# Kernel optimization log

Hardware: AMD Instinct MI355X
Metric: run time of the kernel (lower is better)

Reference implementation:

```python
import jax, jax.numpy as jnp
import numpy as np

N = 16384      # total ligand atoms
E = 65536      # edges
B = 256        # graphs / batch
MAXN = 64      # atoms per graph (max_nodes for to_dense_batch)
FIN = 64       # num_node_features
HID = 256      # hidden_channels
GH = 2         # gat heads
LP = 1024      # protein length
NH = 4         # cross-attention heads
HD = HID // NH
VOCAB = 22


def setup_inputs() -> dict:
    key = jax.random.key(0)
    ks = jax.random.split(key, 48)
    f = jnp.float32
    def nrm(k, shape, s=0.05):
        return jax.random.normal(k, shape, f) * s
    inp = {}
    inp["x"] = jax.random.normal(ks[0], (N, FIN), f)
    inp["edge_index"] = jax.random.randint(ks[1], (2, E), 0, N)
    inp["batch"] = jnp.arange(N) // MAXN  # sorted, 64 atoms per graph
    inp["protein_seq"] = jax.random.randint(ks[2], (B, LP), 0, VOCAB)
    # GAT layer 1 (FIN -> HID, GH heads, concat=False)
    inp["w1"] = nrm(ks[3], (FIN, GH * HID)); inp["as1"] = nrm(ks[4], (GH, HID)); inp["ad1"] = nrm(ks[5], (GH, HID)); inp["b1"] = jnp.zeros((HID,), f)
    inp["w2"] = nrm(ks[6], (HID, GH * HID)); inp["as2"] = nrm(ks[7], (GH, HID)); inp["ad2"] = nrm(ks[8], (GH, HID)); inp["b2"] = jnp.zeros((HID,), f)
    inp["w3"] = nrm(ks[9], (HID, GH * HID)); inp["as3"] = nrm(ks[10], (GH, HID)); inp["ad3"] = nrm(ks[11], (GH, HID)); inp["b3"] = jnp.zeros((HID,), f)
    # protein embedding + conv1d (OIH layout)
    inp["emb"] = nrm(ks[12], (VOCAB, HID), 0.1)
    inp["conv_w"] = nrm(ks[13], (HID, HID, 3)); inp["conv_b"] = jnp.zeros((HID,), f)
    # cross-attention MHA
    inp["wq"] = nrm(ks[14], (HID, HID)); inp["bq"] = jnp.zeros((HID,), f)
    inp["wk"] = nrm(ks[15], (HID, HID)); inp["bk"] = jnp.zeros((HID,), f)
    inp["wv"] = nrm(ks[16], (HID, HID)); inp["bv"] = jnp.zeros((HID,), f)
    inp["wo"] = nrm(ks[17], (HID, HID)); inp["bo"] = jnp.zeros((HID,), f)
    inp["ln1_g"] = jnp.ones((HID,), f); inp["ln1_b"] = jnp.zeros((HID,), f)
    inp["ffw1"] = nrm(ks[18], (HID, 4 * HID)); inp["ffb1"] = jnp.zeros((4 * HID,), f)
    inp["ffw2"] = nrm(ks[19], (4 * HID, HID)); inp["ffb2"] = jnp.zeros((HID,), f)
    inp["ln2_g"] = jnp.ones((HID,), f); inp["ln2_b"] = jnp.zeros((HID,), f)
    inp["fc1_w"] = nrm(ks[20], (HID, HID)); inp["fc1_b"] = jnp.zeros((HID,), f)
    inp["fc2_w"] = nrm(ks[21], (HID, 1)); inp["fc2_b"] = jnp.zeros((1,), f)
    return inp


def _gat(x, edge_index, W, a_src, a_dst, bias):
    # PyG GATConv, concat=False (mean over heads), add_self_loops=True
    n = x.shape[0]
    h = (x @ W).reshape(n, GH, HID)                      # [N,GH,C]
    loop = jnp.arange(n)
    src = jnp.concatenate([edge_index[0], loop])
    dst = jnp.concatenate([edge_index[1], loop])
    a_s = jnp.einsum('nhc,hc->nh', h, a_src)             # [N,GH]
    a_d = jnp.einsum('nhc,hc->nh', h, a_dst)
    e = jax.nn.leaky_relu(a_s[src] + a_d[dst], 0.2)      # [E+N,GH]
    emax = jax.ops.segment_max(e, dst, num_segments=n)   # each node has a self-loop
    ex = jnp.exp(e - emax[dst])
    den = jax.ops.segment_sum(ex, dst, num_segments=n)
    alpha = ex / den[dst]                                # [E+N,GH]
    msg = h[src] * alpha[:, :, None]
    out = jax.ops.segment_sum(msg, dst, num_segments=n)  # [N,GH,C]
    return out.mean(axis=1) + bias


def _to_dense_batch(x, batch):
    # batch is sorted node->graph ids; counts per graph <= MAXN
    ones = jnp.ones((x.shape[0],), jnp.int32)
    counts = jax.ops.segment_sum(ones, batch, num_segments=B)
    starts = jnp.cumsum(counts) - counts
    pos = jnp.arange(x.shape[0]) - starts[batch]
    dense = jnp.zeros((B, MAXN, x.shape[1]), x.dtype).at[batch, pos].set(x)
    mask = jnp.zeros((B, MAXN), bool).at[batch, pos].set(True)
    return dense, mask


def _layernorm(x, g, b, eps=1e-5):
    mu = x.mean(-1, keepdims=True)
    var = ((x - mu) ** 2).mean(-1, keepdims=True)
    return (x - mu) * jax.lax.rsqrt(var + eps) * g + b


def reference(x, edge_index, batch, protein_seq,
              w1, as1, ad1, b1, w2, as2, ad2, b2, w3, as3, ad3, b3,
              emb, conv_w, conv_b,
              wq, bq, wk, bk, wv, bv, wo, bo,
              ln1_g, ln1_b, ffw1, ffb1, ffw2, ffb2, ln2_g, ln2_b,
              fc1_w, fc1_b, fc2_w, fc2_b):
    # --- ligand GNN (eval mode: dropout = identity) ---
    h = jax.nn.elu(_gat(x, edge_index, w1, as1, ad1, b1))
    h = jax.nn.elu(_gat(h, edge_index, w2, as2, ad2, b2))
    h = jax.nn.elu(_gat(h, edge_index, w3, as3, ad3, b3))
    lig, lig_mask = _to_dense_batch(h, batch)            # [B,MAXN,HID], [B,MAXN]
    # --- protein branch ---
    p = emb[protein_seq]                                 # [B,LP,HID]
    p = p.transpose(0, 2, 1)                             # [B,HID,LP]
    p = jax.lax.conv_general_dilated(p, conv_w, (1,), [(1, 1)],
                                     dimension_numbers=('NCH', 'OIH', 'NCH'))
    p = jax.nn.relu(p + conv_b[None, :, None]).transpose(0, 2, 1)  # [B,LP,HID]
    kpm = protein_seq == 0                               # key padding mask
    # --- cross attention (query=ligand, key/value=protein) ---
    q = (lig @ wq + bq).reshape(B, MAXN, NH, HD)
    k = (p @ wk + bk).reshape(B, LP, NH, HD)
    v = (p @ wv + bv).reshape(B, LP, NH, HD)
    scores = jnp.einsum('bqhd,bkhd->bhqk', q, k) / np.sqrt(HD).astype(np.float32)
    scores = jnp.where(kpm[:, None, None, :], jnp.float32(-1e9), scores)
    attn = jax.nn.softmax(scores, axis=-1)               # [B,NH,MAXN,LP]
    ctx = jnp.einsum('bhqk,bkhd->bqhd', attn, v).reshape(B, MAXN, HID)
    attn_out = ctx @ wo + bo
    y = _layernorm(lig + attn_out, ln1_g, ln1_b)
    ff = jax.nn.gelu(y @ ffw1 + ffb1, approximate=False) @ ffw2 + ffb2
    y = _layernorm(y + ff, ln2_g, ln2_b)
    # --- masked mean pool ---
    m = lig_mask[:, :, None].astype(y.dtype)
    pooled = (y * m).sum(axis=1) / (m.sum(axis=1) + 1e-6)
    out = jax.nn.relu(pooled @ fc1_w + fc1_b)
    return out @ fc2_w + fc2_b                           # [B,1]
```

## Files before the change

### kernel.cpp

```cpp
#include <hip/hip_runtime.h>
#include <hip/hip_bf16.h>
#include <cstdint>
#include <cstddef>

#define NAT 16384
#define NED 65536
#define BGR 256
#define FIN 64
#define HID 256
#define LPN 1024
#define HD 64
#define NTRIP 11638
#define NTAB  11648

typedef __bf16 bf16x8 __attribute__((ext_vector_type(8)));
typedef float floatx4 __attribute__((ext_vector_type(4)));

__device__ __forceinline__ void gl2lds16(const void* g, void* l)
{
    __builtin_amdgcn_global_load_lds(
        (const __attribute__((address_space(1))) unsigned int*)g,
        (__attribute__((address_space(3))) unsigned int*)l, 16, 0, 0);
}

template<int ACT, int OUTBF16, int BIASROW>
__global__ __launch_bounds__(512) void gemm_mfma(const __bf16* __restrict__ A,
    const __bf16* __restrict__ Bt, const float* __restrict__ bias,
    void* __restrict__ Cout, int M, int Nn, int K, float escale)
{
    __shared__ __bf16 As[2][128][32];
    __shared__ __bf16 Bs[2][128][32];
    const int t = threadIdx.x;
    const int m0 = blockIdx.y * 128, n0 = blockIdx.x * 128;
    const int w = t >> 6, lane = t & 63;
    const int wm = (w & 3) * 32, wn = (w >> 2) * 64;
    const int quad = lane >> 4, l16 = lane & 15;
    const int r0 = t >> 2, s0 = t & 3, g0 = (s0 ^ (r0 & 3)) * 8;
    const int fso = (quad ^ (l16 & 3)) * 8;
    floatx4 acc[2][4] = {};
    for (int k0 = 0; k0 < K; k0 += 64) {
        gl2lds16(A + (size_t)(m0 + r0) * K + k0 + g0,       &As[0][r0][s0 * 8]);
        gl2lds16(A + (size_t)(m0 + r0) * K + k0 + 32 + g0,  &As[1][r0][s0 * 8]);
        gl2lds16(Bt + (size_t)(n0 + r0) * K + k0 + g0,      &Bs[0][r0][s0 * 8]);
        gl2lds16(Bt + (size_t)(n0 + r0) * K + k0 + 32 + g0, &Bs[1][r0][s0 * 8]);
        __syncthreads();
#pragma unroll
        for (int c = 0; c < 2; c++) {
            bf16x8 af[2], bfr[4];
#pragma unroll
            for (int mi = 0; mi < 2; mi++) af[mi]  = *(const bf16x8*)&As[c][wm + mi * 16 + l16][fso];
#pragma unroll
            for (int nj = 0; nj < 4; nj++) bfr[nj] = *(const bf16x8*)&Bs[c][wn + nj * 16 + l16][fso];
#pragma unroll
            for (int mi = 0; mi < 2; mi++)
#pragma unroll
                for (int nj = 0; nj < 4; nj++)
                    acc[mi][nj] = __builtin_amdgcn_mfma_f32_16x16x32_bf16(af[mi], bfr[nj], acc[mi][nj], 0, 0, 0);
        }
        __syncthreads();
    }
#pragma unroll
    for (int mi = 0; mi < 2; mi++)
#pragma unroll
        for (int nj = 0; nj < 4; nj++) {
            int col = n0 + wn + nj * 16 + l16;
#pragma unroll
            for (int r = 0; r < 4; r++) {
                int row = m0 + wm + mi * 16 + quad * 4 + r;
                float bval = bias ? (BIASROW ? bias[row] : bias[col]) : 0.f;
                float v = (acc[mi][nj][r] + bval) * escale;
                if (ACT == 1) v = fmaxf(v, 0.f);
                if (ACT == 2) v = 0.5f * v * (1.f + erff(v * 0.70710678118654752f));
                if (OUTBF16) ((__bf16*)Cout)[(size_t)row * Nn + col] = (__bf16)v;
                else         ((float*)Cout)[(size_t)row * Nn + col] = v;
            }
        }
}

__global__ __launch_bounds__(512) void gemm_gat(const __bf16* __restrict__ A,
    const __bf16* __restrict__ Bt, const float* __restrict__ as_f,
    const float* __restrict__ ad_f, __bf16* __restrict__ Hg,
    float* __restrict__ part, int K)
{
    __shared__ __bf16 As[2][128][32];
    __shared__ __bf16 Bs[2][128][32];
    const int t = threadIdx.x;
    const int m0 = blockIdx.y * 128, n0 = blockIdx.x * 128;
    const int w = t >> 6, lane = t & 63;
    const int wm = (w & 3) * 32, wn = (w >> 2) * 64;
    const int quad = lane >> 4, l16 = lane & 15;
    const int r0 = t >> 2, s0 = t & 3, g0 = (s0 ^ (r0 & 3)) * 8;
    const int fso = (quad ^ (l16 & 3)) * 8;
    floatx4 acc[2][4] = {};
    for (int k0 = 0; k0 < K; k0 += 64) {
        gl2lds16(A + (size_t)(m0 + r0) * K + k0 + g0,       &As[0][r0][s0 * 8]);
        gl2lds16(A + (size_t)(m0 + r0) * K + k0 + 32 + g0,  &As[1][r0][s0 * 8]);
        gl2lds16(Bt + (size_t)(n0 + r0) * K + k0 + g0,      &Bs[0][r0][s0 * 8]);
        gl2lds16(Bt + (size_t)(n0 + r0) * K + k0 + 32 + g0, &Bs[1][r0][s0 * 8]);
        __syncthreads();
#pragma unroll
        for (int c = 0; c < 2; c++) {
            bf16x8 af[2], bfr[4];
#pragma unroll
            for (int mi = 0; mi < 2; mi++) af[mi]  = *(const bf16x8*)&As[c][wm + mi * 16 + l16][fso];
#pragma unroll
            for (int nj = 0; nj < 4; nj++) bfr[nj] = *(const bf16x8*)&Bs[c][wn + nj * 16 + l16][fso];
#pragma unroll
            for (int mi = 0; mi < 2; mi++)
#pragma unroll
                for (int nj = 0; nj < 4; nj++)
                    acc[mi][nj] = __builtin_amdgcn_mfma_f32_16x16x32_bf16(af[mi], bfr[nj], acc[mi][nj], 0, 0, 0);
        }
        __syncthreads();
    }
    const int slot = blockIdx.x * 2 + (w >> 2);
#pragma unroll
    for (int mi = 0; mi < 2; mi++) {
#pragma unroll
        for (int r = 0; r < 4; r++) {
            float ps = 0.f, pd = 0.f;
#pragma unroll
            for (int nj = 0; nj < 4; nj++) {
                int col = n0 + wn + nj * 16 + l16;
                float v = acc[mi][nj][r];
                ps += v * as_f[col];
                pd += v * ad_f[col];
            }
#pragma unroll
            for (int off = 1; off < 16; off <<= 1) {
                ps += __shfl_xor(ps, off, 64);
                pd += __shfl_xor(pd, off, 64);
            }
            if (l16 == 0) {
                int row = m0 + wm + mi * 16 + quad * 4 + r;
                part[(size_t)(slot * 2 + 0) * NAT + row] = ps;
                part[(size_t)(slot * 2 + 1) * NAT + row] = pd;
            }
        }
    }
#pragma unroll
    for (int mi = 0; mi < 2; mi++)
#pragma unroll
        for (int nj = 0; nj < 4; nj++) {
            int col = n0 + wn + nj * 16 + l16;
#pragma unroll
            for (int r = 0; r < 4; r++) {
                int row = m0 + wm + mi * 16 + quad * 4 + r;
                Hg[(size_t)row * 512 + col] = (__bf16)acc[mi][nj][r];
            }
        }
}

__global__ void fold_k(const float* __restrict__ part, float* __restrict__ a_s,
                       float* __restrict__ a_d)
{
    int n = blockIdx.x * 256 + threadIdx.x;
    float s0 = 0.f, d0 = 0.f, s1 = 0.f, d1 = 0.f;
#pragma unroll
    for (int sl = 0; sl < 4; sl++) {
        s0 += part[(size_t)(sl * 2 + 0) * NAT + n];
        d0 += part[(size_t)(sl * 2 + 1) * NAT + n];
        s1 += part[(size_t)((sl + 4) * 2 + 0) * NAT + n];
        d1 += part[(size_t)((sl + 4) * 2 + 1) * NAT + n];
    }
    a_s[n * 2 + 0] = s0; a_s[n * 2 + 1] = s1;
    a_d[n * 2 + 0] = d0; a_d[n * 2 + 1] = d1;
}

__global__ __launch_bounds__(256) void tap_k(const float* __restrict__ emb,
    const float* __restrict__ cw, float* __restrict__ tap)
{
    const int dlv = blockIdx.x >> 2, part = blockIdx.x & 3;
    const int dl = dlv / 22, v = dlv % 22;
    const int n = threadIdx.x;
    const float* er = emb + v * 256 + part * 64;
    const float* wr = cw + (size_t)n * 768 + part * 192 + dl;
    float s = 0.f;
    for (int k = 0; k < 64; k += 4) {
        s += er[k + 0] * wr[k * 3 + 0];
        s += er[k + 1] * wr[k * 3 + 3];
        s += er[k + 2] * wr[k * 3 + 6];
        s += er[k + 3] * wr[k * 3 + 9];
    }
    atomicAdd(&tap[(size_t)dlv * 256 + n], s);
}

__global__ __launch_bounds__(256) void ptab_k(const float* __restrict__ tap,
    const float* __restrict__ bias, __bf16* __restrict__ P)
{
    const int t = threadIdx.x;
    const int row = blockIdx.x * 8 + (t >> 5);
    const int c = (t & 31) * 8;
    __bf16 o[8];
    if (row < NTRIP) {
        const int a = row / 506, rem = row - a * 506;
        const int t1 = rem / 23, c2 = rem - t1 * 23;
        float acc[8];
#pragma unroll
        for (int j = 0; j < 8; j++) acc[j] = bias[c + j];
        if (a > 0) {
            const float* r = tap + (size_t)(0 * 22 + (a - 1)) * 256 + c;
#pragma unroll
            for (int j = 0; j < 8; j++) acc[j] += r[j];
        }
        {
            const float* r = tap + (size_t)(1 * 22 + t1) * 256 + c;
#pragma unroll
            for (int j = 0; j < 8; j++) acc[j] += r[j];
        }
        if (c2 > 0) {
            const float* r = tap + (size_t)(2 * 22 + (c2 - 1)) * 256 + c;
#pragma unroll
            for (int j = 0; j < 8; j++) acc[j] += r[j];
        }
#pragma unroll
        for (int j = 0; j < 8; j++) o[j] = (__bf16)fmaxf(acc[j], 0.f);
    } else {
#pragma unroll
        for (int j = 0; j < 8; j++) o[j] = (__bf16)0.f;
    }
    *(uint4*)(P + (size_t)row * 256 + c) = *(uint4*)o;
}

__global__ void tid_k(const int* __restrict__ seq, unsigned short* __restrict__ tid)
{
    int i = blockIdx.x * 256 + threadIdx.x;
    int b = i >> 10, l = i & 1023;
    const int* sr = seq + b * LPN;
    int t0 = (l > 0) ? sr[l - 1] : -1;
    int t1 = sr[l];
    int t2 = (l < LPN - 1) ? sr[l + 1] : -1;
    int v = (t0 + 1) * 506 + t1 * 23 + (t2 + 1);
    tid[i] = (unsigned short)(v | (t1 == 0 ? 0x8000 : 0));
}

struct Segs {
    const float* src[12];
    __bf16* dst[12];
    int kdim[12];
    int ndim[12];
    int mode[12];
    int start[13];
};

__global__ void cvtall_k(Segs S, int total)
{
    int i = blockIdx.x * 256 + threadIdx.x;
    if (i >= total) return;
    int s = 0;
    while (i >= S.start[s + 1]) s++;
    int j = i - S.start[s];
    if (S.mode[s] == 0) {
        S.dst[s][j] = (__bf16)S.src[s][j];
    } else {
        int K = S.kdim[s], N = S.ndim[s];
        int n = j / K, k = j - n * K;
        S.dst[s][j] = (__bf16)S.src[s][(size_t)k * N + n];
    }
}

__global__ void deg_k(const int* __restrict__ ei, int* __restrict__ deg)
{
    int e = blockIdx.x * 256 + threadIdx.x;
    if (e < NED) atomicAdd(&deg[ei[NED + e]], 1);
}

__global__ __launch_bounds__(256) void scan_k(const int* __restrict__ deg, int* __restrict__ rowptr)
{
    __shared__ int part[256];
    int t = threadIdx.x;
    int base = t * 64;
    int s = 0;
#pragma unroll
    for (int i = 0; i < 64; i++) s += deg[base + i];
    part[t] = s;
    __syncthreads();
    for (int off = 1; off < 256; off <<= 1) {
        int v = (t >= off) ? part[t - off] : 0;
        __syncthreads();
        part[t] += v;
        __syncthreads();
    }
    int run = t ? part[t - 1] : 0;
    for (int i = 0; i < 64; i++) { rowptr[base + i] = run; run += deg[base + i]; }
    if (t == 255) rowptr[16384] = run;
}

__global__ void scat_k(const int* __restrict__ ei, int* __restrict__ fill,
                       const int* __restrict__ rowptr, int* __restrict__ csrc,
                       int* __restrict__ cdst)
{
    int e = blockIdx.x * 256 + threadIdx.x;
    if (e >= NED) return;
    int d = ei[NED + e];
    int pos = rowptr[d] + atomicAdd(&fill[d], 1);
    csrc[pos] = ei[e];
    cdst[pos] = d;
}

__global__ void erec_k(const int* __restrict__ csrc, const int* __restrict__ cdst,
    const float* __restrict__ a_s, const float* __restrict__ a_d,
    float4* __restrict__ rec)
{
    int p = blockIdx.x * 256 + threadIdx.x;
    if (p >= NED) return;
    int s = csrc[p], d = cdst[p];
    float2 as2 = *(const float2*)(a_s + s * 2);
    float2 ad2 = *(const float2*)(a_d + d * 2);
    float e0 = as2.x + ad2.x; e0 = (e0 > 0.f) ? e0 : 0.2f * e0;
    float e1 = as2.y + ad2.y; e1 = (e1 > 0.f) ? e1 : 0.2f * e1;
    rec[p] = make_float4(e0, e1, __int_as_float(s), 0.f);
}

__global__ __launch_bounds__(256) void gat_agg(const int* __restrict__ rowptr,
    const float4* __restrict__ rec, const __bf16* __restrict__ hgb,
    const float* __restrict__ a_s, const float* __restrict__ a_d,
    const float* __restrict__ bias, float* __restrict__ out, __bf16* __restrict__ outb)
{
    const int wave = threadIdx.x >> 6, lane = threadIdx.x & 63;
    const int d = blockIdx.x * 4 + wave;
    const int beg = rowptr[d], end = rowptr[d + 1];
    float2 as2 = *(const float2*)(a_s + d * 2);
    float2 ad2 = *(const float2*)(a_d + d * 2);
    float e0 = as2.x + ad2.x; e0 = (e0 > 0.f) ? e0 : 0.2f * e0;
    float e1 = as2.y + ad2.y; e1 = (e1 > 0.f) ? e1 : 0.2f * e1;
    float m0 = e0, den0 = 1.f, m1 = e1, den1 = 1.f;
    for (int p = beg; p < end; p++) {
        float4 rc = rec[p];
        float nm0 = fmaxf(m0, rc.x);
        den0 = den0 * __expf(m0 - nm0) + __expf(rc.x - nm0);
        m0 = nm0;
        float nm1 = fmaxf(m1, rc.y);
        den1 = den1 * __expf(m1 - nm1) + __expf(rc.y - nm1);
        m1 = nm1;
    }
    const float inv0 = 1.f / den0, inv1 = 1.f / den1;
    const int ch = lane * 8;
    const int g = ch >> 8;
    const float mg = g ? m1 : m0, invg = g ? inv1 : inv0;
    float acc[8] = {};
    {
        float al = __expf((g ? e1 : e0) - mg) * invg;
        bf16x8 hv = *(const bf16x8*)(hgb + (size_t)d * 512 + ch);
#pragma unroll
        for (int j = 0; j < 8; j++) acc[j] += (float)hv[j] * al;
    }
    for (int p = beg; p < end; p++) {
        float4 rc = rec[p];
        float al = __expf((g ? rc.y : rc.x) - mg) * invg;
        int s = __float_as_int(rc.z);
        bf16x8 hv = *(const bf16x8*)(hgb + (size_t)s * 512 + ch);
#pragma unroll
        for (int j = 0; j < 8; j++) acc[j] += (float)hv[j] * al;
    }
    float other[8];
#pragma unroll
    for (int j = 0; j < 8; j++) other[j] = __shfl_xor(acc[j], 32, 64);
    if (lane < 32) {
#pragma unroll
        for (int j = 0; j < 8; j++) {
            float v = 0.5f * (acc[j] + other[j]) + bias[ch + j];
            v = (v > 0.f) ? v : expm1f(v);
            if (out) out[(size_t)d * 256 + ch + j] = v;
            outb[(size_t)d * 256 + ch + j] = (__bf16)v;
        }
    }
}

__global__ __launch_bounds__(256) void attn4_k(const __bf16* __restrict__ Qb,
    const __bf16* __restrict__ Ktab, const __bf16* __restrict__ Vtab,
    const unsigned short* __restrict__ tid16, __bf16* __restrict__ O)
{
    __shared__ __bf16 Vs[2][4096];
    __shared__ __bf16 Ps[4][16][72];
    __shared__ unsigned short tids[1024];
    const int t = threadIdx.x;
    const int b = blockIdx.x >> 2, h = blockIdx.x & 3;
    const int w = t >> 6, lane = t & 63;
    const int quad = lane >> 4, l16 = lane & 15;
    {
        const uint32_t* src = (const uint32_t*)(tid16 + (size_t)b * LPN);
        ((uint32_t*)tids)[t] = src[t];
        ((uint32_t*)tids)[t + 256] = src[t + 256];
    }
    const __bf16* qrow = Qb + (size_t)(b * 64 + w * 16 + l16) * HID + h * HD;
    bf16x8 aq0 = *(const bf16x8*)(qrow + quad * 8);
    bf16x8 aq1 = *(const bf16x8*)(qrow + 32 + quad * 8);
    __syncthreads();

    auto stageV = [&](int kt, int buf) {
#pragma unroll
        for (int it = 0; it < 2; it++) {
            const int ch0 = (w + it * 4) * 8;
            const int row = tids[kt * 64 + lane] & 0x7fff;
            bf16x8 v = *(const bf16x8*)(Vtab + (size_t)row * 256 + h * HD + ch0);
#pragma unroll
            for (int j = 0; j < 8; j++) {
                const int chl = ch0 + j;
                Vs[buf][chl * 64 + (((lane >> 3) ^ (chl & 7)) << 3) + (lane & 7)] = v[j];
            }
        }
    };

    stageV(0, 0);
    float m_run[4] = {-3e38f, -3e38f, -3e38f, -3e38f};
    float l_run[4] = {0.f, 0.f, 0.f, 0.f};
    floatx4 ctx[4] = {};
    __syncthreads();

    for (int kt = 0; kt < 16; kt++) {
        const int buf = kt & 1;
        if (kt < 15) stageV(kt + 1, buf ^ 1);
        const int kp0 = kt * 64;
        unsigned short tnj[4];
#pragma unroll
        for (int nj = 0; nj < 4; nj++) tnj[nj] = tids[kp0 + nj * 16 + l16];
        floatx4 s[4];
#pragma unroll
        for (int nj = 0; nj < 4; nj++) {
            const __bf16* krow = Ktab + (size_t)(tnj[nj] & 0x7fff) * HID + h * HD;
            bf16x8 bk0 = *(const bf16x8*)(krow + quad * 8);
            bf16x8 bk1 = *(const bf16x8*)(krow + 32 + quad * 8);
            floatx4 z = {0.f, 0.f, 0.f, 0.f};
            s[nj] = __builtin_amdgcn_mfma_f32_16x16x32_bf16(aq0, bk0, z, 0, 0, 0);
            s[nj] = __builtin_amdgcn_mfma_f32_16x16x32_bf16(aq1, bk1, s[nj], 0, 0, 0);
        }
#pragma unroll
        for (int nj = 0; nj < 4; nj++) {
            float mval = (tnj[nj] & 0x8000) ? -1e9f : 0.f;
#pragma unroll
            for (int r = 0; r < 4; r++) s[nj][r] += mval;
        }
        float alpha[4];
#pragma unroll
        for (int r = 0; r < 4; r++) {
            float mx = fmaxf(fmaxf(s[0][r], s[1][r]), fmaxf(s[2][r], s[3][r]));
#pragma unroll
            for (int off = 1; off < 16; off <<= 1) mx = fmaxf(mx, __shfl_xor(mx, off, 64));
            float mn = fmaxf(m_run[r], mx);
            alpha[r] = __expf(m_run[r] - mn);
            m_run[r] = mn;
            float rs = 0.f;
#pragma unroll
            for (int nj = 0; nj < 4; nj++) {
                float p = __expf(s[nj][r] - mn);
                s[nj][r] = p;
                rs += p;
            }
#pragma unroll
            for (int off = 1; off < 16; off <<= 1) rs += __shfl_xor(rs, off, 64);
            l_run[r] = l_run[r] * alpha[r] + rs;
        }
#pragma unroll
        for (int nj = 0; nj < 4; nj++)
#pragma unroll
            for (int r = 0; r < 4; r++)
                Ps[w][quad * 4 + r][nj * 16 + l16] = (__bf16)s[nj][r];
        bf16x8 pa0 = *(const bf16x8*)&Ps[w][l16][quad * 8];
        bf16x8 pa1 = *(const bf16x8*)&Ps[w][l16][32 + quad * 8];
#pragma unroll
        for (int dj = 0; dj < 4; dj++) {
#pragma unroll
            for (int r = 0; r < 4; r++) ctx[dj][r] *= alpha[r];
            const int chl = dj * 16 + l16;
            bf16x8 bv0 = *(const bf16x8*)&Vs[buf][chl * 64 + ((quad ^ (chl & 7)) << 3)];
            bf16x8 bv1 = *(const bf16x8*)&Vs[buf][chl * 64 + (((quad + 4) ^ (chl & 7)) << 3)];
            ctx[dj] = __builtin_amdgcn_mfma_f32_16x16x32_bf16(pa0, bv0, ctx[dj], 0, 0, 0);
            ctx[dj] = __builtin_amdgcn_mfma_f32_16x16x32_bf16(pa1, bv1, ctx[dj], 0, 0, 0);
        }
        __syncthreads();
    }
#pragma unroll
    for (int dj = 0; dj < 4; dj++)
#pragma unroll
        for (int r = 0; r < 4; r++) {
            int q = w * 16 + quad * 4 + r;
            O[((size_t)(b * 64 + q)) * 256 + h * HD + dj * 16 + l16] = (__bf16)(ctx[dj][r] / l_run[r]);
        }
}

__device__ __forceinline__ float blockSum256(float v, float* red)
{
#pragma unroll
    for (int off = 32; off >= 1; off >>= 1) v += __shfl_down(v, off, 64);
    int wave = threadIdx.x >> 6, lane = threadIdx.x & 63;
    if (lane == 0) red[wave] = v;
    __syncthreads();
    float s = red[0] + red[1] + red[2] + red[3];
    __syncthreads();
    return s;
}

__global__ __launch_bounds__(256) void lnres_k(const float* __restrict__ A,
    const float* __restrict__ Bb, const float* __restrict__ g,
    const float* __restrict__ be, float* __restrict__ Y, __bf16* __restrict__ Yb)
{
    __shared__ float red[4];
    int r = blockIdx.x, t = threadIdx.x;
    float v = A[(size_t)r * 256 + t] + Bb[(size_t)r * 256 + t];
    float mean = blockSum256(v, red) * (1.f / 256.f);
    float d = v - mean;
    float var = blockSum256(d * d, red) * (1.f / 256.f);
    float o = d * rsqrtf(var + 1e-5f) * g[t] + be[t];
    Y[(size_t)r * 256 + t] = o;
    if (Yb) Yb[(size_t)r * 256 + t] = (__bf16)o;
}

__global__ __launch_bounds__(256) void head_k(const float* __restrict__ Y,
    const float* __restrict__ fc1w, const float* __restrict__ fc1b,
    const float* __restrict__ fc2w, const float* __restrict__ fc2b,
    float* __restrict__ out)
{
    __shared__ float pooled[256];
    __shared__ float h[256];
    __shared__ float red[4];
    int b = blockIdx.x, t = threadIdx.x;
    float s = 0.f;
#pragma unroll 8
    for (int q = 0; q < 64; q++) s += Y[(size_t)(b * 64 + q) * 256 + t];
    pooled[t] = s / (64.f + 1e-6f);
    __syncthreads();
    float a = 0.f;
    for (int k = 0; k < 256; k += 4) {
        a += pooled[k + 0] * fc1w[(k + 0) * 256 + t];
        a += pooled[k + 1] * fc1w[(k + 1) * 256 + t];
        a += pooled[k + 2] * fc1w[(k + 2) * 256 + t];
        a += pooled[k + 3] * fc1w[(k + 3) * 256 + t];
    }
    h[t] = fmaxf(a + fc1b[t], 0.f);
    __syncthreads();
    float p = h[t] * fc2w[t];
    p = blockSum256(p, red);
    if (t == 0) out[b] = p + fc2b[0];
}

extern "C" void kernel_launch(void* const* d_in, const int* in_sizes, int n_in,
                              void* d_out, int out_size, void* d_ws, size_t ws_size,
                              hipStream_t stream)
{
    const float* x     = (const float*)d_in[0];
    const int*   ei    = (const int*)d_in[1];
    const int*   pseq  = (const int*)d_in[3];
    const float* w1  = (const float*)d_in[4];
    const float* as1 = (const float*)d_in[5];
    const float* ad1 = (const float*)d_in[6];
    const float* b1  = (const float*)d_in[7];
    const float* w2  = (const float*)d_in[8];
    const float* as2 = (const float*)d_in[9];
    const float* ad2 = (const float*)d_in[10];
    const float* b2  = (const float*)d_in[11];
    const float* w3  = (const float*)d_in[12];
    const float* as3 = (const float*)d_in[13];
    const float* ad3 = (const float*)d_in[14];
    const float* b3  = (const float*)d_in[15];
    const float* emb    = (const float*)d_in[16];
    const float* conv_w = (const float*)d_in[17];
    const float* conv_b = (const float*)d_in[18];
    const float* wq = (const float*)d_in[19];
    const float* bq = (const float*)d_in[20];
    const float* wk = (const float*)d_in[21];
    const float* bk = (const float*)d_in[22];
    const float* wv = (const float*)d_in[23];
    const float* bv = (const float*)d_in[24];
    const float* wo = (const float*)d_in[25];
    const float* bo = (const float*)d_in[26];
    const float* ln1_g = (const float*)d_in[27];
    const float* ln1_b = (const float*)d_in[28];
    const float* ffw1  = (const float*)d_in[29];
    const float* ffb1  = (const float*)d_in[30];
    const float* ffw2  = (const float*)d_in[31];
    const float* ffb2  = (const float*)d_in[32];
    const float* ln2_g = (const float*)d_in[33];
    const float* ln2_b = (const float*)d_in[34];
    const float* fc1_w = (const float*)d_in[35];
    const float* fc1_b = (const float*)d_in[36];
    const float* fc2_w = (const float*)d_in[37];
    const float* fc2_b = (const float*)d_in[38];
    (void)in_sizes; (void)n_in; (void)out_size;

    char* ws = (char*)d_ws;
    size_t off = 0;
    auto alloc = [&](size_t bytes) -> char* {
        char* p = ws + off;
        off += (bytes + 255) & ~(size_t)255;
        return p;
    };
    __bf16* hgb  = (__bf16*)alloc((size_t)NAT * 512 * 2);
    float* og    = (float*)alloc((size_t)NAT * 512 * 4);
    float* hb0   = (float*)alloc((size_t)NAT * 256 * 4);
    float* hb1   = (float*)alloc((size_t)NAT * 256 * 4);
    __bf16* xb   = (__bf16*)alloc((size_t)NAT * FIN * 2);
    __bf16* hbb  = (__bf16*)alloc((size_t)NAT * 256 * 2);
    __bf16* qbb  = (__bf16*)alloc((size_t)NAT * 256 * 2);
    __bf16* ctxbb= (__bf16*)alloc((size_t)NAT * 256 * 2);
    __bf16* ybb  = (__bf16*)alloc((size_t)NAT * 256 * 2);
    float* a_s   = (float*)alloc((size_t)NAT * 2 * 4);
    float* a_d   = (float*)alloc((size_t)NAT * 2 * 4);
    float* asd_p = (float*)alloc((size_t)16 * NAT * 4);
    int* deg     = (int*)alloc((size_t)NAT * 4);
    int* fill    = (int*)alloc((size_t)NAT * 4);
    int* rowptr  = (int*)alloc((size_t)(NAT + 1) * 4);
    int* csrc    = (int*)alloc((size_t)NED * 4);
    int* cdst    = (int*)alloc((size_t)NED * 4);
    float4* erec = (float4*)alloc((size_t)NED * 16);
    float* tap   = (float*)alloc((size_t)3 * 22 * 256 * 4);
    __bf16* ptab = (__bf16*)alloc((size_t)NTAB * 256 * 2);
    __bf16* Ktab = (__bf16*)alloc((size_t)NTAB * 256 * 2);
    __bf16* Vtab = (__bf16*)alloc((size_t)NTAB * 256 * 2);
    unsigned short* tid16 = (unsigned short*)alloc((size_t)BGR * LPN * 2);
    __bf16* w1T  = (__bf16*)alloc((size_t)512 * 64 * 2);
    __bf16* w2T  = (__bf16*)alloc((size_t)512 * 256 * 2);
    __bf16* w3T  = (__bf16*)alloc((size_t)512 * 256 * 2);
    __bf16* wkT  = (__bf16*)alloc((size_t)256 * 256 * 2);
    __bf16* wvT  = (__bf16*)alloc((size_t)256 * 256 * 2);
    __bf16* wqT  = (__bf16*)alloc((size_t)256 * 256 * 2);
    __bf16* woT  = (__bf16*)alloc((size_t)256 * 256 * 2);
    __bf16* f1T  = (__bf16*)alloc((size_t)1024 * 256 * 2);
    __bf16* f2T  = (__bf16*)alloc((size_t)256 * 1024 * 2);
    size_t fixed_end = off;
    char* region   = ws + fixed_end;
    __bf16* ffbb   = (__bf16*)region;
    float*  y2     = (float*)(region + (size_t)NAT * 1024 * 2);
    float* attno = og;
    float* ybuf  = og + (size_t)NAT * 256;
    float* ff2o  = hb1;
    (void)ws_size;

    hipMemsetAsync(deg, 0, (size_t)NAT * 8, stream);
    hipMemsetAsync(tap, 0, (size_t)3 * 22 * 256 * 4, stream);
    deg_k<<<NED / 256, 256, 0, stream>>>(ei, deg);
    scan_k<<<1, 256, 0, stream>>>(deg, rowptr);
    scat_k<<<NED / 256, 256, 0, stream>>>(ei, fill, rowptr, csrc, cdst);
    tap_k<<<264, 256, 0, stream>>>(emb, conv_w, tap);

    {
        Segs S;
        const float* srcs[10] = {x, w1, w2, w3, wk, wv, wq, wo, ffw1, ffw2};
        __bf16* dsts[10] = {xb, w1T, w2T, w3T, wkT, wvT, wqT, woT, f1T, f2T};
        int kd[10] = {0, 64, 256, 256, 256, 256, 256, 256, 256, 1024};
        int nd[10] = {0, 512, 512, 512, 256, 256, 256, 256, 1024, 256};
        int md[10] = {0, 1, 1, 1, 1, 1, 1, 1, 1, 1};
        int cnt[10] = {NAT * FIN, 32768, 131072, 131072,
                       65536, 65536, 65536, 65536, 262144, 262144};
        int run = 0;
        for (int i = 0; i < 10; i++) {
            S.src[i] = srcs[i]; S.dst[i] = dsts[i];
            S.kdim[i] = kd[i]; S.ndim[i] = nd[i]; S.mode[i] = md[i];
            S.start[i] = run; run += cnt[i];
        }
        S.start[10] = run; S.start[11] = run; S.start[12] = run;
        cvtall_k<<<(run + 255) / 256, 256, 0, stream>>>(S, run);
    }

    ptab_k<<<NTAB / 8, 256, 0, stream>>>(tap, conv_b, ptab);
    tid_k<<<BGR * LPN / 256, 256, 0, stream>>>(pseq, tid16);
    gemm_mfma<0, 1, 0><<<dim3(2, NTAB / 128), 512, 0, stream>>>(ptab, wkT, bk, Ktab, NTAB, 256, 256, 1.f);
    gemm_mfma<0, 1, 0><<<dim3(2, NTAB / 128), 512, 0, stream>>>(ptab, wvT, bv, Vtab, NTAB, 256, 256, 1.f);

    const __bf16* WT[3] = {w1T, w2T, w3T};
    const float* asl[3] = {as1, as2, as3};
    const float* adl[3] = {ad1, ad2, ad3};
    const float* bl[3]  = {b1, b2, b3};
    float* houts[3] = {nullptr, nullptr, hb0};
    const __bf16* hinb = xb;
    int Kdim = FIN;
    for (int l = 0; l < 3; l++) {
        gemm_gat<<<dim3(4, NAT / 128), 512, 0, stream>>>(hinb, WT[l], asl[l], adl[l], hgb, asd_p, Kdim);
        fold_k<<<NAT / 256, 256, 0, stream>>>(asd_p, a_s, a_d);
        erec_k<<<NED / 256, 256, 0, stream>>>(csrc, cdst, a_s, a_d, erec);
        gat_agg<<<NAT / 4, 256, 0, stream>>>(rowptr, erec, hgb, a_s, a_d, bl[l], houts[l], hbb);
        hinb = hbb;
        Kdim = HID;
    }
    const float* lig = hb0;
    const __bf16* ligb = hbb;

    gemm_mfma<0, 1, 0><<<dim3(2, NAT / 128), 512, 0, stream>>>(ligb, wqT, bq, qbb, NAT, 256, 256, 0.125f);

    attn4_k<<<BGR * 4, 256, 0, stream>>>(qbb, Ktab, Vtab, tid16, ctxbb);

    gemm_mfma<0, 0, 0><<<dim3(2, NAT / 128), 512, 0, stream>>>(ctxbb, woT, bo, attno, NAT, 256, 256, 1.f);
    lnres_k<<<NAT, 256, 0, stream>>>(lig, attno, ln1_g, ln1_b, ybuf, ybb);
    gemm_mfma<2, 1, 0><<<dim3(8, NAT / 128), 512, 0, stream>>>(ybb, f1T, ffb1, ffbb, NAT, 1024, 256, 1.f);
    gemm_mfma<0, 0, 0><<<dim3(2, NAT / 128), 512, 0, stream>>>(ffbb, f2T, ffb2, ff2o, NAT, 256, 1024, 1.f);
    lnres_k<<<NAT, 256, 0, stream>>>(ybuf, ff2o, ln2_g, ln2_b, y2, nullptr);

    head_k<<<BGR, 256, 0, stream>>>(y2, fc1_w, fc1_b, fc2_w, fc2_b, (float*)d_out);
}
```

Measured before the change: 540.4 us.

## Head-split K/V tables, register-prefetch V and K, reorder attention blocks

The K/V projection GEMMs now write their tables head-major ([head][row][64]), so each attention head reads a compact 64-wide slice instead of striding through 256-wide rows. In the attention kernel, the V tile for the next step is loaded into registers early and written to LDS only after the MFMA work, and K rows are loaded into registers ahead of the score MFMAs. This is meant to hide gather latency behind compute. Block indices are remapped so that pairs of batches share a head in nearby blocks, and the kernel gets a launch bound of 4 blocks per SIMD/CU. The trade-off is higher register pressure from holding the prefetched K and V values.

```diff
diff --git a/kernel.cpp b/kernel.cpp
--- a/kernel.cpp
+++ b/kernel.cpp
@@ -23,7 +23,7 @@
         (__attribute__((address_space(3))) unsigned int*)l, 16, 0, 0);
 }
 
-template<int ACT, int OUTBF16, int BIASROW>
+template<int ACT, int OUTBF16, int BIASROW, int HSPLIT>
 __global__ __launch_bounds__(512) void gemm_mfma(const __bf16* __restrict__ A,
     const __bf16* __restrict__ Bt, const float* __restrict__ bias,
     void* __restrict__ Cout, int M, int Nn, int K, float escale)
@@ -71,8 +71,9 @@
                 float v = (acc[mi][nj][r] + bval) * escale;
                 if (ACT == 1) v = fmaxf(v, 0.f);
                 if (ACT == 2) v = 0.5f * v * (1.f + erff(v * 0.70710678118654752f));
-                if (OUTBF16) ((__bf16*)Cout)[(size_t)row * Nn + col] = (__bf16)v;
-                else         ((float*)Cout)[(size_t)row * Nn + col] = v;
+                if (HSPLIT)      ((__bf16*)Cout)[((size_t)(col >> 6) * M + row) * 64 + (col & 63)] = (__bf16)v;
+                else if (OUTBF16) ((__bf16*)Cout)[(size_t)row * Nn + col] = (__bf16)v;
+                else              ((float*)Cout)[(size_t)row * Nn + col] = v;
             }
         }
 }
@@ -367,7 +368,7 @@
     }
 }
 
-__global__ __launch_bounds__(256) void attn4_k(const __bf16* __restrict__ Qb,
+__global__ __launch_bounds__(256, 4) void attn4_k(const __bf16* __restrict__ Qb,
     const __bf16* __restrict__ Ktab, const __bf16* __restrict__ Vtab,
     const unsigned short* __restrict__ tid16, __bf16* __restrict__ O)
 {
@@ -375,9 +376,13 @@
     __shared__ __bf16 Ps[4][16][72];
     __shared__ unsigned short tids[1024];
     const int t = threadIdx.x;
-    const int b = blockIdx.x >> 2, h = blockIdx.x & 3;
+    const int bid = blockIdx.x;
+    const int h = (bid >> 1) & 3;
+    const int b = ((bid >> 3) << 1) | (bid & 1);
     const int w = t >> 6, lane = t & 63;
     const int quad = lane >> 4, l16 = lane & 15;
+    const __bf16* Kh = Ktab + (size_t)h * NTAB * 64;
+    const __bf16* Vh = Vtab + (size_t)h * NTAB * 64;
     {
         const uint32_t* src = (const uint32_t*)(tid16 + (size_t)b * LPN);
         ((uint32_t*)tids)[t] = src[t];
@@ -388,21 +393,29 @@
     bf16x8 aq1 = *(const bf16x8*)(qrow + 32 + quad * 8);
     __syncthreads();
 
-    auto stageV = [&](int kt, int buf) {
+    auto loadV = [&](int kt, bf16x8* vr) {
 #pragma unroll
         for (int it = 0; it < 2; it++) {
             const int ch0 = (w + it * 4) * 8;
             const int row = tids[kt * 64 + lane] & 0x7fff;
-            bf16x8 v = *(const bf16x8*)(Vtab + (size_t)row * 256 + h * HD + ch0);
+            vr[it] = *(const bf16x8*)(Vh + (size_t)row * 64 + ch0);
+        }
+    };
+    auto writeV = [&](const bf16x8* vr, int buf) {
+#pragma unroll
+        for (int it = 0; it < 2; it++) {
+            const int ch0 = (w + it * 4) * 8;
 #pragma unroll
             for (int j = 0; j < 8; j++) {
                 const int chl = ch0 + j;
-                Vs[buf][chl * 64 + (((lane >> 3) ^ (chl & 7)) << 3) + (lane & 7)] = v[j];
+                Vs[buf][chl * 64 + (((lane >> 3) ^ (chl & 7)) << 3) + (lane & 7)] = vr[it][j];
             }
         }
     };
 
-    stageV(0, 0);
+    bf16x8 vr[2];
+    loadV(0, vr);
+    writeV(vr, 0);
     float m_run[4] = {-3e38f, -3e38f, -3e38f, -3e38f};
     float l_run[4] = {0.f, 0.f, 0.f, 0.f};
     floatx4 ctx[4] = {};
@@ -410,20 +423,23 @@
 
     for (int kt = 0; kt < 16; kt++) {
         const int buf = kt & 1;
-        if (kt < 15) stageV(kt + 1, buf ^ 1);
         const int kp0 = kt * 64;
         unsigned short tnj[4];
-#pragma unroll
-        for (int nj = 0; nj < 4; nj++) tnj[nj] = tids[kp0 + nj * 16 + l16];
+        bf16x8 kc0[4], kc1[4];
+#pragma unroll
+        for (int nj = 0; nj < 4; nj++) {
+            tnj[nj] = tids[kp0 + nj * 16 + l16];
+            const __bf16* krow = Kh + (size_t)(tnj[nj] & 0x7fff) * 64;
+            kc0[nj] = *(const bf16x8*)(krow + quad * 8);
+            kc1[nj] = *(const bf16x8*)(krow + 32 + quad * 8);
+        }
+        if (kt < 15) loadV(kt + 1, vr);
         floatx4 s[4];
 #pragma unroll
         for (int nj = 0; nj < 4; nj++) {
-            const __bf16* krow = Ktab + (size_t)(tnj[nj] & 0x7fff) * HID + h * HD;
-            bf16x8 bk0 = *(const bf16x8*)(krow + quad * 8);
-            bf16x8 bk1 = *(const bf16x8*)(krow + 32 + quad * 8);
             floatx4 z = {0.f, 0.f, 0.f, 0.f};
-            s[nj] = __builtin_amdgcn_mfma_f32_16x16x32_bf16(aq0, bk0, z, 0, 0, 0);
-            s[nj] = __builtin_amdgcn_mfma_f32_16x16x32_bf16(aq1, bk1, s[nj], 0, 0, 0);
+            s[nj] = __builtin_amdgcn_mfma_f32_16x16x32_bf16(aq0, kc0[nj], z, 0, 0, 0);
+            s[nj] = __builtin_amdgcn_mfma_f32_16x16x32_bf16(aq1, kc1[nj], s[nj], 0, 0, 0);
         }
 #pragma unroll
         for (int nj = 0; nj < 4; nj++) {
@@ -468,6 +484,7 @@
             ctx[dj] = __builtin_amdgcn_mfma_f32_16x16x32_bf16(pa0, bv0, ctx[dj], 0, 0, 0);
             ctx[dj] = __builtin_amdgcn_mfma_f32_16x16x32_bf16(pa1, bv1, ctx[dj], 0, 0, 0);
         }
+        if (kt < 15) writeV(vr, buf ^ 1);
         __syncthreads();
     }
 #pragma unroll
@@ -654,8 +671,8 @@
 
     ptab_k<<<NTAB / 8, 256, 0, stream>>>(tap, conv_b, ptab);
     tid_k<<<BGR * LPN / 256, 256, 0, stream>>>(pseq, tid16);
-    gemm_mfma<0, 1, 0><<<dim3(2, NTAB / 128), 512, 0, stream>>>(ptab, wkT, bk, Ktab, NTAB, 256, 256, 1.f);
-    gemm_mfma<0, 1, 0><<<dim3(2, NTAB / 128), 512, 0, stream>>>(ptab, wvT, bv, Vtab, NTAB, 256, 256, 1.f);
+    gemm_mfma<0, 1, 0, 1><<<dim3(2, NTAB / 128), 512, 0, stream>>>(ptab, wkT, bk, Ktab, NTAB, 256, 256, 1.f);
+    gemm_mfma<0, 1, 0, 1><<<dim3(2, NTAB / 128), 512, 0, stream>>>(ptab, wvT, bv, Vtab, NTAB, 256, 256, 1.f);
 
     const __bf16* WT[3] = {w1T, w2T, w3T};
     const float* asl[3] = {as1, as2, as3};
@@ -675,14 +692,14 @@
     const float* lig = hb0;
     const __bf16* ligb = hbb;
 
-    gemm_mfma<0, 1, 0><<<dim3(2, NAT / 128), 512, 0, stream>>>(ligb, wqT, bq, qbb, NAT, 256, 256, 0.125f);
+    gemm_mfma<0, 1, 0, 0><<<dim3(2, NAT / 128), 512, 0, stream>>>(ligb, wqT, bq, qbb, NAT, 256, 256, 0.125f);
 
     attn4_k<<<BGR * 4, 256, 0, stream>>>(qbb, Ktab, Vtab, tid16, ctxbb);
 
-    gemm_mfma<0, 0, 0><<<dim3(2, NAT / 128), 512, 0, stream>>>(ctxbb, woT, bo, attno, NAT, 256, 256, 1.f);
+    gemm_mfma<0, 0, 0, 0><<<dim3(2, NAT / 128), 512, 0, stream>>>(ctxbb, woT, bo, attno, NAT, 256, 256, 1.f);
     lnres_k<<<NAT, 256, 0, stream>>>(lig, attno, ln1_g, ln1_b, ybuf, ybb);
-    gemm_mfma<2, 1, 0><<<dim3(8, NAT / 128), 512, 0, stream>>>(ybb, f1T, ffb1, ffbb, NAT, 1024, 256, 1.f);
-    gemm_mfma<0, 0, 0><<<dim3(2, NAT / 128), 512, 0, stream>>>(ffbb, f2T, ffb2, ff2o, NAT, 256, 1024, 1.f);
+    gemm_mfma<2, 1, 0, 0><<<dim3(8, NAT / 128), 512, 0, stream>>>(ybb, f1T, ffb1, ffbb, NAT, 1024, 256, 1.f);
+    gemm_mfma<0, 0, 0, 0><<<dim3(2, NAT / 128), 512, 0, stream>>>(ffbb, f2T, ffb2, ff2o, NAT, 256, 1024, 1.f);
     lnres_k<<<NAT, 256, 0, stream>>>(ybuf, ff2o, ln2_g, ln2_b, y2, nullptr);
 
     head_k<<<BGR, 256, 0, stream>>>(y2, fc1_w, fc1_b, fc2_w, fc2_b, (float*)d_out);
```

New measurement: 541.9 us. No clear change (+0.3%).
